# Kernel tuning notes

Hardware: AMD Instinct MI355X
Metric: run time of the kernel (lower is better)

The kernel has to match this reference:

```python
import jax, jax.numpy as jnp
import numpy as np

# Multi-scale feature pyramid (H, W) per level, standard Deformable-DETR for ~800x800 input
SHAPES = [(100, 100), (50, 50), (25, 25), (13, 13)]
D = 256      # d_model
NH = 8       # n_heads
NL = 4       # n_levels
NP = 4       # n_points
HD = D // NH # head_dim = 32
B = 2
S = sum(h * w for h, w in SHAPES)  # 13294
Lq = S  # encoder-style: one query per multi-scale token


def setup_inputs() -> dict:
    key = jax.random.key(0)
    ks = jax.random.split(key, 11)
    return {
        "query": jax.random.normal(ks[0], (B, Lq, D), jnp.float32),
        "reference_points": jax.random.uniform(ks[1], (B, Lq, NL, 2), jnp.float32),
        "value": jax.random.normal(ks[2], (B, S, D), jnp.float32),
        "W_val": jax.random.normal(ks[3], (D, D), jnp.float32) * 0.02,
        "b_val": jnp.zeros((D,), jnp.float32),
        "W_off": jax.random.normal(ks[4], (D, NH * NL * NP * 2), jnp.float32) * 0.01,
        "b_off": jax.random.normal(ks[5], (NH * NL * NP * 2,), jnp.float32) * 0.5,
        "W_attn": jax.random.normal(ks[6], (D, NH * NL * NP), jnp.float32) * 0.02,
        "b_attn": jnp.zeros((NH * NL * NP,), jnp.float32),
        "W_out": jax.random.normal(ks[7], (D, D), jnp.float32) * 0.02,
        "b_out": jnp.zeros((D,), jnp.float32),
    }


def _bilinear_sample(valf, x, y, H, W):
    """grid_sample(mode=bilinear, padding_mode=zeros, align_corners=False).
    valf: [N, H*W, C] flattened feature map; x, y: [N, P] pixel-space coords
    (already converted via x = loc_x*W - 0.5). Returns [N, P, C].
    """
    x0 = jnp.floor(x); y0 = jnp.floor(y)
    x1 = x0 + 1.0;     y1 = y0 + 1.0
    wx1 = x - x0; wx0 = 1.0 - wx1
    wy1 = y - y0; wy0 = 1.0 - wy1

    def corner(xi, yi, w):
        inb = (xi >= 0) & (xi <= W - 1) & (yi >= 0) & (yi <= H - 1)
        xi_c = jnp.clip(xi, 0, W - 1).astype(jnp.int32)
        yi_c = jnp.clip(yi, 0, H - 1).astype(jnp.int32)
        idx = yi_c * W + xi_c                                   # [N, P]
        v = jnp.take_along_axis(valf, idx[..., None], axis=1)   # [N, P, C]
        return v * (w * inb.astype(valf.dtype))[..., None]

    return (corner(x0, y0, wx0 * wy0) + corner(x1, y0, wx1 * wy0)
            + corner(x0, y1, wx0 * wy1) + corner(x1, y1, wx1 * wy1))


def reference(query, reference_points, value, W_val, b_val, W_off, b_off,
              W_attn, b_attn, W_out, b_out):
    Bq, L, _ = query.shape
    # value projection, split into heads: [B, S, NH, HD]
    val = (value @ W_val + b_val).reshape(Bq, S, NH, HD)
    # sampling offsets and attention weights from query
    offsets = (query @ W_off + b_off).reshape(Bq, L, NH, NL, NP, 2)
    w = (query @ W_attn + b_attn).reshape(Bq, L, NH, NL * NP)
    w = jax.nn.softmax(w, axis=-1).reshape(Bq, L, NH, NL, NP)
    # normalize offsets by (W, H) per level; 2D reference points path
    offset_norm = jnp.array([[wd, h] for h, wd in SHAPES], jnp.float32)  # [NL, 2]
    locs = (reference_points[:, :, None, :, None, :]
            + offsets / offset_norm[None, None, None, :, None, :])       # [B,L,NH,NL,NP,2]

    splits = [h * wd for h, wd in SHAPES]
    starts = np.concatenate([[0], np.cumsum(splits)])
    out_acc = jnp.zeros((Bq, L, NH, HD), query.dtype)
    for lvl, (H, W) in enumerate(SHAPES):
        vl = val[:, starts[lvl]:starts[lvl + 1]]                 # [B, HW, NH, HD]
        vl = vl.transpose(0, 2, 1, 3).reshape(Bq * NH, H * W, HD)
        loc = locs[:, :, :, lvl].transpose(0, 2, 1, 3, 4).reshape(Bq * NH, L * NP, 2)
        x = loc[..., 0] * W - 0.5   # align_corners=False pixel coords
        y = loc[..., 1] * H - 0.5
        s = _bilinear_sample(vl, x, y, H, W).reshape(Bq, NH, L, NP, HD)
        wl = w[:, :, :, lvl].transpose(0, 2, 1, 3)               # [B, NH, L, NP]
        out_acc = out_acc + jnp.einsum('bhqpd,bhqp->bqhd', s, wl)
    out = out_acc.reshape(Bq, L, NH * HD)
    return out @ W_out + b_out
```

## Files before the change

### kernel.cpp

```cpp
#include <hip/hip_runtime.h>
#include <hip/hip_bf16.h>
#include <math.h>

#define B_    2
#define D_    256
#define NH_   8
#define NL_   4
#define NP_   4
#define HD_   32
#define S_    13294
#define L_    13294
#define M_    (B_ * L_)

__device__ __constant__ int c_H[NL_]     = {100, 50, 25, 13};
__device__ __constant__ int c_W[NL_]     = {100, 50, 25, 13};
__device__ __constant__ int c_start[NL_] = {0, 10000, 12500, 13125};

typedef __attribute__((ext_vector_type(8))) short  short8;
typedef __attribute__((ext_vector_type(4))) float  float4v;

__device__ __forceinline__ unsigned short f2bf(float f) {
    unsigned u = __float_as_uint(f);
    unsigned r = 0x7fffu + ((u >> 16) & 1u);
    return (unsigned short)((u + r) >> 16);
}
__device__ __forceinline__ float bflo(int u) {
    return __uint_as_float((unsigned)u << 16);
}
__device__ __forceinline__ float bfhi(int u) {
    return __uint_as_float((unsigned)u & 0xffff0000u);
}

__global__ __launch_bounds__(256) void prep_weights(
    const float* __restrict__ W_val, const float* __restrict__ W_off,
    const float* __restrict__ W_attn, const float* __restrict__ b_off,
    const float* __restrict__ b_attn, const float* __restrict__ W_out,
    unsigned short* __restrict__ wt_val, unsigned short* __restrict__ wt_oa,
    unsigned short* __restrict__ wt_out, float* __restrict__ bias_oa)
{
    int i = blockIdx.x * 256 + threadIdx.x;
    if (i < 65536) {
        int n = i >> 8, k = i & 255;
        wt_val[i] = f2bf(W_val[k * 256 + n]);
    } else if (i < 65536 + 98304) {
        int j = i - 65536;
        int n = j >> 8, k = j & 255;
        float v = (n < 256) ? W_off[k * 256 + n] : W_attn[k * 128 + (n - 256)];
        wt_oa[j] = f2bf(v);
    } else if (i < 65536 + 98304 + 65536) {
        int j = i - 163840;
        int n = j >> 8, k = j & 255;
        wt_out[j] = f2bf(W_out[k * 256 + n]);
    } else if (i < 229376 + 384) {
        int j = i - 229376;
        bias_oa[j] = (j < 256) ? b_off[j] : b_attn[j - 256];
    }
}

template <bool A_F32, bool OUT_BF16>
__global__ __launch_bounds__(256) void gemm_mfma(
    const void* __restrict__ Av,
    const unsigned short* __restrict__ WT,
    const float* __restrict__ bias,
    void* __restrict__ Cv,
    int M, int N)
{
    __shared__ unsigned short As[128][40];
    __shared__ unsigned short Bs[128][40];

    const int tid  = threadIdx.x;
    const int lane = tid & 63;
    const int wave = tid >> 6;
    const int rowBase = blockIdx.x * 128;
    const int colBase = blockIdx.y * 128;
    const int wm = (wave >> 1) * 64;
    const int wn = (wave & 1) * 64;

    float4v acc[4][4] = {};

    const int fr = lane & 15;
    const int fk = (lane >> 4) * 8;

    for (int k0 = 0; k0 < 256; k0 += 32) {
        __syncthreads();
#pragma unroll
        for (int i = 0; i < 2; ++i) {
            const int c  = tid + i * 256;
            const int r  = c >> 2;
            const int ko = (c & 3) * 8;
            const int gr = rowBase + r;
            short8 va = {};
            if (gr < M) {
                if constexpr (A_F32) {
                    const float* Ap = (const float*)Av + (size_t)gr * 256 + k0 + ko;
                    float4 f0 = *reinterpret_cast<const float4*>(Ap);
                    float4 f1 = *reinterpret_cast<const float4*>(Ap + 4);
                    va[0] = (short)f2bf(f0.x); va[1] = (short)f2bf(f0.y);
                    va[2] = (short)f2bf(f0.z); va[3] = (short)f2bf(f0.w);
                    va[4] = (short)f2bf(f1.x); va[5] = (short)f2bf(f1.y);
                    va[6] = (short)f2bf(f1.z); va[7] = (short)f2bf(f1.w);
                } else {
                    va = *reinterpret_cast<const short8*>(
                        (const unsigned short*)Av + (size_t)gr * 256 + k0 + ko);
                }
            }
            *reinterpret_cast<short8*>(&As[r][ko]) = va;
            const int gc = colBase + r;
            short8 vb = *reinterpret_cast<const short8*>(WT + (size_t)gc * 256 + k0 + ko);
            *reinterpret_cast<short8*>(&Bs[r][ko]) = vb;
        }
        __syncthreads();

        short8 af[4], bf[4];
#pragma unroll
        for (int t = 0; t < 4; ++t) {
            af[t] = *reinterpret_cast<const short8*>(&As[wm + t * 16 + fr][fk]);
            bf[t] = *reinterpret_cast<const short8*>(&Bs[wn + t * 16 + fr][fk]);
        }
#pragma unroll
        for (int mt = 0; mt < 4; ++mt)
#pragma unroll
            for (int nt = 0; nt < 4; ++nt)
                acc[mt][nt] = __builtin_amdgcn_mfma_f32_16x16x32_bf16(
                    af[mt], bf[nt], acc[mt][nt], 0, 0, 0);
    }

    const int dn  = lane & 15;
    const int dm0 = (lane >> 4) * 4;
#pragma unroll
    for (int mt = 0; mt < 4; ++mt) {
#pragma unroll
        for (int nt = 0; nt < 4; ++nt) {
            const int col = colBase + wn + nt * 16 + dn;
            const float bv = bias[col];
#pragma unroll
            for (int r = 0; r < 4; ++r) {
                const int row = rowBase + wm + mt * 16 + dm0 + r;
                if (row < M) {
                    const float v = acc[mt][nt][r] + bv;
                    if constexpr (OUT_BF16)
                        ((unsigned short*)Cv)[(size_t)row * N + col] = f2bf(v);
                    else
                        ((float*)Cv)[(size_t)row * N + col] = v;
                }
            }
        }
    }
}

__global__ __launch_bounds__(256) void deform_sample_v2(
    const unsigned short* __restrict__ val,
    const float* __restrict__ refp,
    const float* __restrict__ oa,
    unsigned short* __restrict__ acc)
{
    const int tid = threadIdx.x;
    const int q0  = blockIdx.x * 8;

    __shared__ float sLog[8][128];
    __shared__ int2  sPack[8][4][16][9];

    {
        const int q  = tid >> 5;
        const int f  = tid & 31;
        const int bq = min(q0 + q, M_ - 1);
        float4 v = *reinterpret_cast<const float4*>(oa + (size_t)bq * 384 + 256 + f * 4);
        *reinterpret_cast<float4*>(&sLog[q][f * 4]) = v;
    }
    __syncthreads();

#pragma unroll
    for (int k = 0; k < 4; ++k) {
        const int e   = tid + k * 256;
        const int q   = e >> 7;
        const int t   = e & 127;
        const int h   = t >> 4;
        const int lp  = t & 15;
        const int lvl = lp >> 2;
        const int p   = lp & 3;
        const int bq  = min(q0 + q, M_ - 1);

        float m = -1e30f;
#pragma unroll
        for (int i = 0; i < 16; ++i) m = fmaxf(m, sLog[q][h * 16 + i]);
        float s = 0.f;
#pragma unroll
        for (int i = 0; i < 16; ++i) s += __expf(sLog[q][h * 16 + i] - m);
        const float wgt = __expf(sLog[q][t] - m) / s;

        const int Wi = c_W[lvl], Hi = c_H[lvl], st = c_start[lvl];
        const float rx = refp[((size_t)bq * NL_ + lvl) * 2 + 0];
        const float ry = refp[((size_t)bq * NL_ + lvl) * 2 + 1];
        const float ox = oa[(size_t)bq * 384 + h * 32 + lvl * 8 + p * 2 + 0];
        const float oy = oa[(size_t)bq * 384 + h * 32 + lvl * 8 + p * 2 + 1];
        const float x = rx * (float)Wi + ox - 0.5f;
        const float y = ry * (float)Hi + oy - 0.5f;

        const float x0f = floorf(x), y0f = floorf(y);
        const int   x0 = (int)x0f,   y0 = (int)y0f;
        const float wx1 = x - x0f, wx0 = 1.f - wx1;
        const float wy1 = y - y0f, wy0 = 1.f - wy1;

        const int   cx[4] = {x0, x0 + 1, x0,     x0 + 1};
        const int   cy[4] = {y0, y0,     y0 + 1, y0 + 1};
        const float cw[4] = {wx0 * wy0, wx1 * wy0, wx0 * wy1, wx1 * wy1};
#pragma unroll
        for (int c = 0; c < 4; ++c) {
            const bool inb = (cx[c] >= 0) & (cx[c] < Wi) & (cy[c] >= 0) & (cy[c] < Hi);
            const int xi = min(max(cx[c], 0), Wi - 1);
            const int yi = min(max(cy[c], 0), Hi - 1);
            int2 pk;
            pk.x = st + yi * Wi + xi;
            pk.y = __float_as_int(inb ? wgt * cw[c] : 0.f);
            sPack[q][c][lp][h] = pk;
        }
    }
    __syncthreads();

    const int q  = tid >> 5;
    const int h  = (tid >> 2) & 7;
    const int d4 = tid & 3;
    const int bq = q0 + q;
    const int b  = min(bq, M_ - 1) / L_;
    const unsigned short* vb = val + (size_t)b * S_ * 256 + h * 32 + d4 * 8;

    float a0 = 0, a1 = 0, a2 = 0, a3 = 0, a4 = 0, a5 = 0, a6 = 0, a7 = 0;
#pragma unroll 4
    for (int lp = 0; lp < 16; ++lp) {
#pragma unroll
        for (int c = 0; c < 4; ++c) {
            const int2 pk = sPack[q][c][lp][h];
            const float w = __int_as_float(pk.y);
            const int4 u = *reinterpret_cast<const int4*>(vb + (size_t)pk.x * 256);
            a0 += w * bflo(u.x); a1 += w * bfhi(u.x);
            a2 += w * bflo(u.y); a3 += w * bfhi(u.y);
            a4 += w * bflo(u.z); a5 += w * bfhi(u.z);
            a6 += w * bflo(u.w); a7 += w * bfhi(u.w);
        }
    }
    if (bq < M_) {
        int4 o;
        o.x = (int)f2bf(a0) | ((int)f2bf(a1) << 16);
        o.y = (int)f2bf(a2) | ((int)f2bf(a3) << 16);
        o.z = (int)f2bf(a4) | ((int)f2bf(a5) << 16);
        o.w = (int)f2bf(a6) | ((int)f2bf(a7) << 16);
        *reinterpret_cast<int4*>(acc + (size_t)bq * 256 + h * 32 + d4 * 8) = o;
    }
}

extern "C" void kernel_launch(void* const* d_in, const int* in_sizes, int n_in,
                              void* d_out, int out_size, void* d_ws, size_t ws_size,
                              hipStream_t stream) {
    const float* query  = (const float*)d_in[0];
    const float* refp   = (const float*)d_in[1];
    const float* value  = (const float*)d_in[2];
    const float* W_val  = (const float*)d_in[3];
    const float* b_val  = (const float*)d_in[4];
    const float* W_off  = (const float*)d_in[5];
    const float* b_off  = (const float*)d_in[6];
    const float* W_attn = (const float*)d_in[7];
    const float* b_attn = (const float*)d_in[8];
    const float* W_out  = (const float*)d_in[9];
    const float* b_out  = (const float*)d_in[10];
    float* out = (float*)d_out;

    char* ws = (char*)d_ws;
    const size_t mb = (size_t)M_ * 256;
    unsigned short* val_bf  = (unsigned short*)ws;  ws += mb * 2;
    unsigned short* acc_bf  = (unsigned short*)ws;  ws += mb * 2;
    float*          oa_f    = (float*)ws;           ws += (size_t)M_ * 384 * 4;
    unsigned short* wt_val  = (unsigned short*)ws;  ws += 65536 * 2;
    unsigned short* wt_oa   = (unsigned short*)ws;  ws += 98304 * 2;
    unsigned short* wt_out  = (unsigned short*)ws;  ws += 65536 * 2;
    float*          bias_oa = (float*)ws;           ws += 384 * 4;

    const int M = M_;
    dim3 blk(256);

    prep_weights<<<dim3(898), blk, 0, stream>>>(
        W_val, W_off, W_attn, b_off, b_attn, W_out, wt_val, wt_oa, wt_out, bias_oa);

    const dim3 gV((M + 127) / 128, 2);
    const dim3 gOA((M + 127) / 128, 3);

    gemm_mfma<true, true><<<gV, blk, 0, stream>>>(value, wt_val, b_val, val_bf, M, 256);
    gemm_mfma<true, false><<<gOA, blk, 0, stream>>>(query, wt_oa, bias_oa, oa_f, M, 384);
    deform_sample_v2<<<dim3((M + 7) / 8), blk, 0, stream>>>(val_bf, refp, oa_f, acc_bf);
    gemm_mfma<false, false><<<gV, blk, 0, stream>>>(acc_bf, wt_out, b_out, out, M, 256);
}
```

Measured before the change: 240.0 us.

## Merge value and offset GEMMs into one launch, shrink tiles, pack sample weights as fp16

The value-projection and offset/attention GEMMs now run as a single launch whose grid y-dimension selects the problem. Column tiles shrink from 128 to 64, which doubles the block count. In the sampling kernel the per-head softmax max and sum are computed once per (query, head) instead of once per sample point. Each sample index and its weight are packed into one 32-bit word with the weight stored as fp16, which halves shared-memory traffic but lowers weight precision. The smaller GEMM tiles re-read the A operand more often and give less reuse per block.

```diff
diff --git a/kernel.cpp b/kernel.cpp
--- a/kernel.cpp
+++ b/kernel.cpp
@@ -24,11 +24,15 @@
     unsigned r = 0x7fffu + ((u >> 16) & 1u);
     return (unsigned short)((u + r) >> 16);
 }
-__device__ __forceinline__ float bflo(int u) {
-    return __uint_as_float((unsigned)u << 16);
-}
-__device__ __forceinline__ float bfhi(int u) {
-    return __uint_as_float((unsigned)u & 0xffff0000u);
+__device__ __forceinline__ float bflo(int u) { return __uint_as_float((unsigned)u << 16); }
+__device__ __forceinline__ float bfhi(int u) { return __uint_as_float((unsigned)u & 0xffff0000u); }
+__device__ __forceinline__ unsigned short f2h(float f) {
+    _Float16 h = (_Float16)f;
+    return __builtin_bit_cast(unsigned short, h);
+}
+__device__ __forceinline__ float h2f(unsigned short u) {
+    _Float16 h = __builtin_bit_cast(_Float16, u);
+    return (float)h;
 }
 
 __global__ __launch_bounds__(256) void prep_weights(
@@ -57,27 +61,33 @@
     }
 }
 
-template <bool A_F32, bool OUT_BF16>
-__global__ __launch_bounds__(256) void gemm_mfma(
-    const void* __restrict__ Av,
-    const unsigned short* __restrict__ WT,
-    const float* __restrict__ bias,
-    void* __restrict__ Cv,
-    int M, int N)
+__global__ __launch_bounds__(256) void gemm_fused(
+    const float* __restrict__ value, const float* __restrict__ query,
+    const unsigned short* __restrict__ wt_val, const unsigned short* __restrict__ wt_oa,
+    const float* __restrict__ b_val, const float* __restrict__ bias_oa,
+    unsigned short* __restrict__ val_bf, float* __restrict__ oa_f)
 {
     __shared__ unsigned short As[128][40];
-    __shared__ unsigned short Bs[128][40];
+    __shared__ unsigned short Bs[64][40];
 
     const int tid  = threadIdx.x;
     const int lane = tid & 63;
     const int wave = tid >> 6;
     const int rowBase = blockIdx.x * 128;
-    const int colBase = blockIdx.y * 128;
+    const int y = blockIdx.y;
+
+    const float* A;
+    const unsigned short* WT;
+    const float* bias;
+    int N, colBase;
+    bool outBF16;
+    if (y < 4) { A = value; WT = wt_val; bias = b_val;   N = 256; colBase = y * 64;      outBF16 = true;  }
+    else       { A = query; WT = wt_oa;  bias = bias_oa; N = 384; colBase = (y - 4) * 64; outBF16 = false; }
+
     const int wm = (wave >> 1) * 64;
-    const int wn = (wave & 1) * 64;
-
-    float4v acc[4][4] = {};
-
+    const int wn = (wave & 1) * 32;
+
+    float4v acc[4][2] = {};
     const int fr = lane & 15;
     const int fk = (lane >> 4) * 8;
 
@@ -90,37 +100,119 @@
             const int ko = (c & 3) * 8;
             const int gr = rowBase + r;
             short8 va = {};
-            if (gr < M) {
-                if constexpr (A_F32) {
-                    const float* Ap = (const float*)Av + (size_t)gr * 256 + k0 + ko;
-                    float4 f0 = *reinterpret_cast<const float4*>(Ap);
-                    float4 f1 = *reinterpret_cast<const float4*>(Ap + 4);
-                    va[0] = (short)f2bf(f0.x); va[1] = (short)f2bf(f0.y);
-                    va[2] = (short)f2bf(f0.z); va[3] = (short)f2bf(f0.w);
-                    va[4] = (short)f2bf(f1.x); va[5] = (short)f2bf(f1.y);
-                    va[6] = (short)f2bf(f1.z); va[7] = (short)f2bf(f1.w);
-                } else {
-                    va = *reinterpret_cast<const short8*>(
-                        (const unsigned short*)Av + (size_t)gr * 256 + k0 + ko);
+            if (gr < M_) {
+                const float* Ap = A + (size_t)gr * 256 + k0 + ko;
+                float4 f0 = *reinterpret_cast<const float4*>(Ap);
+                float4 f1 = *reinterpret_cast<const float4*>(Ap + 4);
+                va[0] = (short)f2bf(f0.x); va[1] = (short)f2bf(f0.y);
+                va[2] = (short)f2bf(f0.z); va[3] = (short)f2bf(f0.w);
+                va[4] = (short)f2bf(f1.x); va[5] = (short)f2bf(f1.y);
+                va[6] = (short)f2bf(f1.z); va[7] = (short)f2bf(f1.w);
+            }
+            *reinterpret_cast<short8*>(&As[r][ko]) = va;
+        }
+        {
+            const int r  = tid >> 2;
+            const int ko = (tid & 3) * 8;
+            short8 vb = *reinterpret_cast<const short8*>(
+                WT + (size_t)(colBase + r) * 256 + k0 + ko);
+            *reinterpret_cast<short8*>(&Bs[r][ko]) = vb;
+        }
+        __syncthreads();
+
+        short8 af[4], bf[2];
+#pragma unroll
+        for (int t = 0; t < 4; ++t)
+            af[t] = *reinterpret_cast<const short8*>(&As[wm + t * 16 + fr][fk]);
+#pragma unroll
+        for (int t = 0; t < 2; ++t)
+            bf[t] = *reinterpret_cast<const short8*>(&Bs[wn + t * 16 + fr][fk]);
+#pragma unroll
+        for (int mt = 0; mt < 4; ++mt)
+#pragma unroll
+            for (int nt = 0; nt < 2; ++nt)
+                acc[mt][nt] = __builtin_amdgcn_mfma_f32_16x16x32_bf16(
+                    af[mt], bf[nt], acc[mt][nt], 0, 0, 0);
+    }
+
+    const int dn  = lane & 15;
+    const int dm0 = (lane >> 4) * 4;
+#pragma unroll
+    for (int mt = 0; mt < 4; ++mt) {
+#pragma unroll
+        for (int nt = 0; nt < 2; ++nt) {
+            const int col = colBase + wn + nt * 16 + dn;
+            const float bv = bias[col];
+#pragma unroll
+            for (int r = 0; r < 4; ++r) {
+                const int row = rowBase + wm + mt * 16 + dm0 + r;
+                if (row < M_) {
+                    const float v = acc[mt][nt][r] + bv;
+                    if (outBF16)
+                        val_bf[(size_t)row * 256 + col] = f2bf(v);
+                    else
+                        oa_f[(size_t)row * 384 + col] = v;
                 }
             }
+        }
+    }
+}
+
+__global__ __launch_bounds__(256) void gemm_out(
+    const unsigned short* __restrict__ Abf,
+    const unsigned short* __restrict__ WT,
+    const float* __restrict__ bias,
+    float* __restrict__ C)
+{
+    __shared__ unsigned short As[128][40];
+    __shared__ unsigned short Bs[64][40];
+
+    const int tid  = threadIdx.x;
+    const int lane = tid & 63;
+    const int wave = tid >> 6;
+    const int rowBase = blockIdx.x * 128;
+    const int colBase = blockIdx.y * 64;
+
+    const int wm = (wave >> 1) * 64;
+    const int wn = (wave & 1) * 32;
+
+    float4v acc[4][2] = {};
+    const int fr = lane & 15;
+    const int fk = (lane >> 4) * 8;
+
+    for (int k0 = 0; k0 < 256; k0 += 32) {
+        __syncthreads();
+#pragma unroll
+        for (int i = 0; i < 2; ++i) {
+            const int c  = tid + i * 256;
+            const int r  = c >> 2;
+            const int ko = (c & 3) * 8;
+            const int gr = rowBase + r;
+            short8 va = {};
+            if (gr < M_)
+                va = *reinterpret_cast<const short8*>(Abf + (size_t)gr * 256 + k0 + ko);
             *reinterpret_cast<short8*>(&As[r][ko]) = va;
-            const int gc = colBase + r;
-            short8 vb = *reinterpret_cast<const short8*>(WT + (size_t)gc * 256 + k0 + ko);
+        }
+        {
+            const int r  = tid >> 2;
+            const int ko = (tid & 3) * 8;
+            short8 vb = *reinterpret_cast<const short8*>(
+                WT + (size_t)(colBase + r) * 256 + k0 + ko);
             *reinterpret_cast<short8*>(&Bs[r][ko]) = vb;
         }
         __syncthreads();
 
-        short8 af[4], bf[4];
-#pragma unroll
-        for (int t = 0; t < 4; ++t) {
+        short8 af[4], bf[2];
+#pragma unroll
+        for (int t = 0; t < 4; ++t)
             af[t] = *reinterpret_cast<const short8*>(&As[wm + t * 16 + fr][fk]);
+#pragma unroll
+        for (int t = 0; t < 2; ++t)
             bf[t] = *reinterpret_cast<const short8*>(&Bs[wn + t * 16 + fr][fk]);
-        }
 #pragma unroll
         for (int mt = 0; mt < 4; ++mt)
 #pragma unroll
-            for (int nt = 0; nt < 4; ++nt)
+            for (int nt = 0; nt < 2; ++nt)
                 acc[mt][nt] = __builtin_amdgcn_mfma_f32_16x16x32_bf16(
                     af[mt], bf[nt], acc[mt][nt], 0, 0, 0);
     }
@@ -130,25 +222,20 @@
 #pragma unroll
     for (int mt = 0; mt < 4; ++mt) {
 #pragma unroll
-        for (int nt = 0; nt < 4; ++nt) {
+        for (int nt = 0; nt < 2; ++nt) {
             const int col = colBase + wn + nt * 16 + dn;
             const float bv = bias[col];
 #pragma unroll
             for (int r = 0; r < 4; ++r) {
                 const int row = rowBase + wm + mt * 16 + dm0 + r;
-                if (row < M) {
-                    const float v = acc[mt][nt][r] + bv;
-                    if constexpr (OUT_BF16)
-                        ((unsigned short*)Cv)[(size_t)row * N + col] = f2bf(v);
-                    else
-                        ((float*)Cv)[(size_t)row * N + col] = v;
-                }
+                if (row < M_)
+                    C[(size_t)row * 256 + col] = acc[mt][nt][r] + bv;
             }
         }
     }
 }
 
-__global__ __launch_bounds__(256) void deform_sample_v2(
+__global__ __launch_bounds__(256) void deform_sample_v3(
     const unsigned short* __restrict__ val,
     const float* __restrict__ refp,
     const float* __restrict__ oa,
@@ -158,7 +245,8 @@
     const int q0  = blockIdx.x * 8;
 
     __shared__ float sLog[8][128];
-    __shared__ int2  sPack[8][4][16][9];
+    __shared__ float sMS[8][8][2];
+    __shared__ int   sPack[8][4][16][8];
 
     {
         const int q  = tid >> 5;
@@ -166,6 +254,19 @@
         const int bq = min(q0 + q, M_ - 1);
         float4 v = *reinterpret_cast<const float4*>(oa + (size_t)bq * 384 + 256 + f * 4);
         *reinterpret_cast<float4*>(&sLog[q][f * 4]) = v;
+    }
+    __syncthreads();
+
+    if (tid < 64) {
+        const int q = tid >> 3, h = tid & 7;
+        float m = -1e30f;
+#pragma unroll
+        for (int i = 0; i < 16; ++i) m = fmaxf(m, sLog[q][h * 16 + i]);
+        float s = 0.f;
+#pragma unroll
+        for (int i = 0; i < 16; ++i) s += __expf(sLog[q][h * 16 + i] - m);
+        sMS[q][h][0] = m;
+        sMS[q][h][1] = 1.f / s;
     }
     __syncthreads();
 
@@ -180,13 +281,7 @@
         const int p   = lp & 3;
         const int bq  = min(q0 + q, M_ - 1);
 
-        float m = -1e30f;
-#pragma unroll
-        for (int i = 0; i < 16; ++i) m = fmaxf(m, sLog[q][h * 16 + i]);
-        float s = 0.f;
-#pragma unroll
-        for (int i = 0; i < 16; ++i) s += __expf(sLog[q][h * 16 + i] - m);
-        const float wgt = __expf(sLog[q][t] - m) / s;
+        const float wgt = __expf(sLog[q][t] - sMS[q][h][0]) * sMS[q][h][1];
 
         const int Wi = c_W[lvl], Hi = c_H[lvl], st = c_start[lvl];
         const float rx = refp[((size_t)bq * NL_ + lvl) * 2 + 0];
@@ -209,10 +304,9 @@
             const bool inb = (cx[c] >= 0) & (cx[c] < Wi) & (cy[c] >= 0) & (cy[c] < Hi);
             const int xi = min(max(cx[c], 0), Wi - 1);
             const int yi = min(max(cy[c], 0), Hi - 1);
-            int2 pk;
-            pk.x = st + yi * Wi + xi;
-            pk.y = __float_as_int(inb ? wgt * cw[c] : 0.f);
-            sPack[q][c][lp][h] = pk;
+            const int idx = st + yi * Wi + xi;
+            const unsigned short wh = f2h(inb ? wgt * cw[c] : 0.f);
+            sPack[q][c][lp][h] = idx | ((int)wh << 16);
         }
     }
     __syncthreads();
@@ -225,18 +319,18 @@
     const unsigned short* vb = val + (size_t)b * S_ * 256 + h * 32 + d4 * 8;
 
     float a0 = 0, a1 = 0, a2 = 0, a3 = 0, a4 = 0, a5 = 0, a6 = 0, a7 = 0;
-#pragma unroll 4
-    for (int lp = 0; lp < 16; ++lp) {
-#pragma unroll
-        for (int c = 0; c < 4; ++c) {
-            const int2 pk = sPack[q][c][lp][h];
-            const float w = __int_as_float(pk.y);
-            const int4 u = *reinterpret_cast<const int4*>(vb + (size_t)pk.x * 256);
-            a0 += w * bflo(u.x); a1 += w * bfhi(u.x);
-            a2 += w * bflo(u.y); a3 += w * bfhi(u.y);
-            a4 += w * bflo(u.z); a5 += w * bfhi(u.z);
-            a6 += w * bflo(u.w); a7 += w * bfhi(u.w);
-        }
+#pragma unroll 8
+    for (int i = 0; i < 64; ++i) {
+        const int lp = i >> 2;
+        const int c  = i & 3;
+        const int pk = sPack[q][c][lp][h];
+        const float w = h2f((unsigned short)((unsigned)pk >> 16));
+        const unsigned idx = (unsigned)pk & 0xffffu;
+        const int4 u = *reinterpret_cast<const int4*>(vb + (size_t)idx * 256);
+        a0 += w * bflo(u.x); a1 += w * bfhi(u.x);
+        a2 += w * bflo(u.y); a3 += w * bfhi(u.y);
+        a4 += w * bflo(u.z); a5 += w * bfhi(u.z);
+        a6 += w * bflo(u.w); a7 += w * bfhi(u.w);
     }
     if (bq < M_) {
         int4 o;
@@ -274,17 +368,15 @@
     unsigned short* wt_out  = (unsigned short*)ws;  ws += 65536 * 2;
     float*          bias_oa = (float*)ws;           ws += 384 * 4;
 
-    const int M = M_;
     dim3 blk(256);
 
     prep_weights<<<dim3(898), blk, 0, stream>>>(
         W_val, W_off, W_attn, b_off, b_attn, W_out, wt_val, wt_oa, wt_out, bias_oa);
 
-    const dim3 gV((M + 127) / 128, 2);
-    const dim3 gOA((M + 127) / 128, 3);
-
-    gemm_mfma<true, true><<<gV, blk, 0, stream>>>(value, wt_val, b_val, val_bf, M, 256);
-    gemm_mfma<true, false><<<gOA, blk, 0, stream>>>(query, wt_oa, bias_oa, oa_f, M, 384);
-    deform_sample_v2<<<dim3((M + 7) / 8), blk, 0, stream>>>(val_bf, refp, oa_f, acc_bf);
-    gemm_mfma<false, false><<<gV, blk, 0, stream>>>(acc_bf, wt_out, b_out, out, M, 256);
-}
+    gemm_fused<<<dim3((M_ + 127) / 128, 10), blk, 0, stream>>>(
+        value, query, wt_val, wt_oa, b_val, bias_oa, val_bf, oa_f);
+
+    deform_sample_v3<<<dim3((M_ + 7) / 8), blk, 0, stream>>>(val_bf, refp, oa_f, acc_bf);
+
+    gemm_out<<<dim3((M_ + 127) / 128, 4), blk, 0, stream>>>(acc_bf, wt_out, b_out, out);
+}
```

Measured after the change: 212.2 us. 11.6% less time.

## Merge value/query GEMMs, register-prefetch tiles, fp16 value and packed sample indices

Applied to the files above, without the earlier changes.

The value and offset/attention projections now run in one launch, with a 64-row tile that covers the full output width. A register-prefetched loop loads the next K-slice while the MFMAs run on the current one. The value projection is stored as fp16 instead of bf16. The sampling kernel computes the softmax max and sum once per head rather than once per thread, and packs the 16-bit index with an fp16 weight into one int so the LDS table is smaller. fp16 value storage can overflow or lose range compared with bf16, and the 16-bit index only holds because S is below 65536.

```diff
diff --git a/kernel.cpp b/kernel.cpp
--- a/kernel.cpp
+++ b/kernel.cpp
@@ -3,14 +3,13 @@
 #include <math.h>
 
 #define B_    2
-#define D_    256
 #define NH_   8
 #define NL_   4
 #define NP_   4
 #define HD_   32
 #define S_    13294
 #define L_    13294
-#define M_    (B_ * L_)
+#define M_    26588
 
 __device__ __constant__ int c_H[NL_]     = {100, 50, 25, 13};
 __device__ __constant__ int c_W[NL_]     = {100, 50, 25, 13};
@@ -24,11 +23,13 @@
     unsigned r = 0x7fffu + ((u >> 16) & 1u);
     return (unsigned short)((u + r) >> 16);
 }
-__device__ __forceinline__ float bflo(int u) {
-    return __uint_as_float((unsigned)u << 16);
-}
-__device__ __forceinline__ float bfhi(int u) {
-    return __uint_as_float((unsigned)u & 0xffff0000u);
+__device__ __forceinline__ unsigned short f2h(float f) {
+    _Float16 h = (_Float16)f;
+    return __builtin_bit_cast(unsigned short, h);
+}
+__device__ __forceinline__ float h2f(unsigned short u) {
+    _Float16 h = __builtin_bit_cast(_Float16, u);
+    return (float)h;
 }
 
 __global__ __launch_bounds__(256) void prep_weights(
@@ -57,98 +58,151 @@
     }
 }
 
-template <bool A_F32, bool OUT_BF16>
-__global__ __launch_bounds__(256) void gemm_mfma(
+template<int N, int OUT, bool AF32>
+__device__ __forceinline__ void gemm_body(
     const void* __restrict__ Av,
     const unsigned short* __restrict__ WT,
     const float* __restrict__ bias,
     void* __restrict__ Cv,
-    int M, int N)
-{
-    __shared__ unsigned short As[128][40];
-    __shared__ unsigned short Bs[128][40];
+    unsigned short (* __restrict__ As)[40],
+    unsigned short (* __restrict__ Bs)[40])
+{
+    constexpr int NT  = N / 64;
+    constexpr int NCH = N / 64;
 
     const int tid  = threadIdx.x;
     const int lane = tid & 63;
     const int wave = tid >> 6;
-    const int rowBase = blockIdx.x * 128;
-    const int colBase = blockIdx.y * 128;
-    const int wm = (wave >> 1) * 64;
-    const int wn = (wave & 1) * 64;
-
-    float4v acc[4][4] = {};
+    const int rowBase = blockIdx.x * 64;
+    const int wcol = wave * (N / 4);
+
+    const int ar   = tid >> 2;
+    const int ako  = (tid & 3) * 8;
+    const int grow = rowBase + ar;
+
+    float4v acc[4][NT] = {};
+    float4 pa0, pa1;
+    short8 pah;
+    short8 pb[NCH];
+
+    auto loadAB = [&](int k0) {
+        if constexpr (AF32) {
+            const float* A = (const float*)Av;
+            if (grow < M_) {
+                pa0 = *reinterpret_cast<const float4*>(A + (size_t)grow * 256 + k0 + ako);
+                pa1 = *reinterpret_cast<const float4*>(A + (size_t)grow * 256 + k0 + ako + 4);
+            } else {
+                pa0 = make_float4(0.f, 0.f, 0.f, 0.f); pa1 = pa0;
+            }
+        } else {
+            const unsigned short* A = (const unsigned short*)Av;
+            if (grow < M_)
+                pah = *reinterpret_cast<const short8*>(A + (size_t)grow * 256 + k0 + ako);
+            else
+                pah = short8{};
+        }
+#pragma unroll
+        for (int i = 0; i < NCH; ++i) {
+            const int c = tid + i * 256;
+            pb[i] = *reinterpret_cast<const short8*>(
+                WT + (size_t)(c >> 2) * 256 + k0 + (c & 3) * 8);
+        }
+    };
+
+    auto storeLDS = [&]() {
+        short8 s;
+        if constexpr (AF32) {
+            s[0] = (short)f2bf(pa0.x); s[1] = (short)f2bf(pa0.y);
+            s[2] = (short)f2bf(pa0.z); s[3] = (short)f2bf(pa0.w);
+            s[4] = (short)f2bf(pa1.x); s[5] = (short)f2bf(pa1.y);
+            s[6] = (short)f2bf(pa1.z); s[7] = (short)f2bf(pa1.w);
+        } else {
+            s = pah;
+        }
+        *reinterpret_cast<short8*>(&As[ar][ako]) = s;
+#pragma unroll
+        for (int i = 0; i < NCH; ++i) {
+            const int c = tid + i * 256;
+            *reinterpret_cast<short8*>(&Bs[c >> 2][(c & 3) * 8]) = pb[i];
+        }
+    };
 
     const int fr = lane & 15;
     const int fk = (lane >> 4) * 8;
 
-    for (int k0 = 0; k0 < 256; k0 += 32) {
+    loadAB(0);
+#pragma unroll
+    for (int it = 0; it < 8; ++it) {
         __syncthreads();
-#pragma unroll
-        for (int i = 0; i < 2; ++i) {
-            const int c  = tid + i * 256;
-            const int r  = c >> 2;
-            const int ko = (c & 3) * 8;
-            const int gr = rowBase + r;
-            short8 va = {};
-            if (gr < M) {
-                if constexpr (A_F32) {
-                    const float* Ap = (const float*)Av + (size_t)gr * 256 + k0 + ko;
-                    float4 f0 = *reinterpret_cast<const float4*>(Ap);
-                    float4 f1 = *reinterpret_cast<const float4*>(Ap + 4);
-                    va[0] = (short)f2bf(f0.x); va[1] = (short)f2bf(f0.y);
-                    va[2] = (short)f2bf(f0.z); va[3] = (short)f2bf(f0.w);
-                    va[4] = (short)f2bf(f1.x); va[5] = (short)f2bf(f1.y);
-                    va[6] = (short)f2bf(f1.z); va[7] = (short)f2bf(f1.w);
-                } else {
-                    va = *reinterpret_cast<const short8*>(
-                        (const unsigned short*)Av + (size_t)gr * 256 + k0 + ko);
+        storeLDS();
+        __syncthreads();
+        if (it < 7) loadAB((it + 1) * 32);
+
+        short8 af[4], bf[NT];
+#pragma unroll
+        for (int t = 0; t < 4; ++t)
+            af[t] = *reinterpret_cast<const short8*>(&As[t * 16 + fr][fk]);
+#pragma unroll
+        for (int t = 0; t < NT; ++t)
+            bf[t] = *reinterpret_cast<const short8*>(&Bs[wcol + t * 16 + fr][fk]);
+#pragma unroll
+        for (int mt = 0; mt < 4; ++mt)
+#pragma unroll
+            for (int nt = 0; nt < NT; ++nt)
+                acc[mt][nt] = __builtin_amdgcn_mfma_f32_16x16x32_bf16(
+                    af[mt], bf[nt], acc[mt][nt], 0, 0, 0);
+    }
+
+    const int dn  = lane & 15;
+    const int dm0 = (lane >> 4) * 4;
+#pragma unroll
+    for (int mt = 0; mt < 4; ++mt) {
+#pragma unroll
+        for (int nt = 0; nt < NT; ++nt) {
+            const int col = wcol + nt * 16 + dn;
+            const float bv = bias[col];
+#pragma unroll
+            for (int r = 0; r < 4; ++r) {
+                const int row = rowBase + mt * 16 + dm0 + r;
+                if (row < M_) {
+                    const float v = acc[mt][nt][r] + bv;
+                    if constexpr (OUT == 0)
+                        ((unsigned short*)Cv)[(size_t)row * 256 + col] = f2h(v);
+                    else if constexpr (OUT == 1)
+                        ((float*)Cv)[(size_t)row * 384 + col] = v;
+                    else
+                        ((float*)Cv)[(size_t)row * 256 + col] = v;
                 }
             }
-            *reinterpret_cast<short8*>(&As[r][ko]) = va;
-            const int gc = colBase + r;
-            short8 vb = *reinterpret_cast<const short8*>(WT + (size_t)gc * 256 + k0 + ko);
-            *reinterpret_cast<short8*>(&Bs[r][ko]) = vb;
-        }
-        __syncthreads();
-
-        short8 af[4], bf[4];
-#pragma unroll
-        for (int t = 0; t < 4; ++t) {
-            af[t] = *reinterpret_cast<const short8*>(&As[wm + t * 16 + fr][fk]);
-            bf[t] = *reinterpret_cast<const short8*>(&Bs[wn + t * 16 + fr][fk]);
-        }
-#pragma unroll
-        for (int mt = 0; mt < 4; ++mt)
-#pragma unroll
-            for (int nt = 0; nt < 4; ++nt)
-                acc[mt][nt] = __builtin_amdgcn_mfma_f32_16x16x32_bf16(
-                    af[mt], bf[nt], acc[mt][nt], 0, 0, 0);
-    }
-
-    const int dn  = lane & 15;
-    const int dm0 = (lane >> 4) * 4;
-#pragma unroll
-    for (int mt = 0; mt < 4; ++mt) {
-#pragma unroll
-        for (int nt = 0; nt < 4; ++nt) {
-            const int col = colBase + wn + nt * 16 + dn;
-            const float bv = bias[col];
-#pragma unroll
-            for (int r = 0; r < 4; ++r) {
-                const int row = rowBase + wm + mt * 16 + dm0 + r;
-                if (row < M) {
-                    const float v = acc[mt][nt][r] + bv;
-                    if constexpr (OUT_BF16)
-                        ((unsigned short*)Cv)[(size_t)row * N + col] = f2bf(v);
-                    else
-                        ((float*)Cv)[(size_t)row * N + col] = v;
-                }
-            }
-        }
-    }
-}
-
-__global__ __launch_bounds__(256) void deform_sample_v2(
+        }
+    }
+}
+
+__global__ __launch_bounds__(256) void gemm_vq(
+    const float* __restrict__ value, const float* __restrict__ query,
+    const unsigned short* __restrict__ wt_val, const unsigned short* __restrict__ wt_oa,
+    const float* __restrict__ b_val, const float* __restrict__ bias_oa,
+    unsigned short* __restrict__ val_f16, float* __restrict__ oa_f)
+{
+    __shared__ unsigned short As[64][40];
+    __shared__ unsigned short Bs[384][40];
+    if (blockIdx.y == 0)
+        gemm_body<256, 0, true>(value, wt_val, b_val, val_f16, As, Bs);
+    else
+        gemm_body<384, 1, true>(query, wt_oa, bias_oa, oa_f, As, Bs);
+}
+
+__global__ __launch_bounds__(256) void gemm_out2(
+    const unsigned short* __restrict__ Abf,
+    const unsigned short* __restrict__ WT,
+    const float* __restrict__ bias, float* __restrict__ C)
+{
+    __shared__ unsigned short As[64][40];
+    __shared__ unsigned short Bs[256][40];
+    gemm_body<256, 2, false>(Abf, WT, bias, C, As, Bs);
+}
+
+__global__ __launch_bounds__(256) void deform_sample_v4(
     const unsigned short* __restrict__ val,
     const float* __restrict__ refp,
     const float* __restrict__ oa,
@@ -158,7 +212,8 @@
     const int q0  = blockIdx.x * 8;
 
     __shared__ float sLog[8][128];
-    __shared__ int2  sPack[8][4][16][9];
+    __shared__ float sMS[8][8][2];
+    __shared__ int   sPack[8][4][16][8];
 
     {
         const int q  = tid >> 5;
@@ -166,6 +221,19 @@
         const int bq = min(q0 + q, M_ - 1);
         float4 v = *reinterpret_cast<const float4*>(oa + (size_t)bq * 384 + 256 + f * 4);
         *reinterpret_cast<float4*>(&sLog[q][f * 4]) = v;
+    }
+    __syncthreads();
+
+    if (tid < 64) {
+        const int q = tid >> 3, h = tid & 7;
+        float m = -1e30f;
+#pragma unroll
+        for (int i = 0; i < 16; ++i) m = fmaxf(m, sLog[q][h * 16 + i]);
+        float s = 0.f;
+#pragma unroll
+        for (int i = 0; i < 16; ++i) s += __expf(sLog[q][h * 16 + i] - m);
+        sMS[q][h][0] = m;
+        sMS[q][h][1] = 1.f / s;
     }
     __syncthreads();
 
@@ -180,13 +248,7 @@
         const int p   = lp & 3;
         const int bq  = min(q0 + q, M_ - 1);
 
-        float m = -1e30f;
-#pragma unroll
-        for (int i = 0; i < 16; ++i) m = fmaxf(m, sLog[q][h * 16 + i]);
-        float s = 0.f;
-#pragma unroll
-        for (int i = 0; i < 16; ++i) s += __expf(sLog[q][h * 16 + i] - m);
-        const float wgt = __expf(sLog[q][t] - m) / s;
+        const float wgt = __expf(sLog[q][t] - sMS[q][h][0]) * sMS[q][h][1];
 
         const int Wi = c_W[lvl], Hi = c_H[lvl], st = c_start[lvl];
         const float rx = refp[((size_t)bq * NL_ + lvl) * 2 + 0];
@@ -209,10 +271,9 @@
             const bool inb = (cx[c] >= 0) & (cx[c] < Wi) & (cy[c] >= 0) & (cy[c] < Hi);
             const int xi = min(max(cx[c], 0), Wi - 1);
             const int yi = min(max(cy[c], 0), Hi - 1);
-            int2 pk;
-            pk.x = st + yi * Wi + xi;
-            pk.y = __float_as_int(inb ? wgt * cw[c] : 0.f);
-            sPack[q][c][lp][h] = pk;
+            const int idx = st + yi * Wi + xi;
+            const unsigned short wh = f2h(inb ? wgt * cw[c] : 0.f);
+            sPack[q][c][lp][h] = idx | ((int)wh << 16);
         }
     }
     __syncthreads();
@@ -225,18 +286,22 @@
     const unsigned short* vb = val + (size_t)b * S_ * 256 + h * 32 + d4 * 8;
 
     float a0 = 0, a1 = 0, a2 = 0, a3 = 0, a4 = 0, a5 = 0, a6 = 0, a7 = 0;
-#pragma unroll 4
-    for (int lp = 0; lp < 16; ++lp) {
-#pragma unroll
-        for (int c = 0; c < 4; ++c) {
-            const int2 pk = sPack[q][c][lp][h];
-            const float w = __int_as_float(pk.y);
-            const int4 u = *reinterpret_cast<const int4*>(vb + (size_t)pk.x * 256);
-            a0 += w * bflo(u.x); a1 += w * bfhi(u.x);
-            a2 += w * bflo(u.y); a3 += w * bfhi(u.y);
-            a4 += w * bflo(u.z); a5 += w * bfhi(u.z);
-            a6 += w * bflo(u.w); a7 += w * bfhi(u.w);
-        }
+#pragma unroll 8
+    for (int i = 0; i < 64; ++i) {
+        const int lp = i >> 2;
+        const int c  = i & 3;
+        const int pk = sPack[q][c][lp][h];
+        const float w = h2f((unsigned short)((unsigned)pk >> 16));
+        const unsigned idx = (unsigned)pk & 0xffffu;
+        const int4 u = *reinterpret_cast<const int4*>(vb + (size_t)idx * 256);
+        a0 += w * h2f((unsigned short)(u.x & 0xffff));
+        a1 += w * h2f((unsigned short)((unsigned)u.x >> 16));
+        a2 += w * h2f((unsigned short)(u.y & 0xffff));
+        a3 += w * h2f((unsigned short)((unsigned)u.y >> 16));
+        a4 += w * h2f((unsigned short)(u.z & 0xffff));
+        a5 += w * h2f((unsigned short)((unsigned)u.z >> 16));
+        a6 += w * h2f((unsigned short)(u.w & 0xffff));
+        a7 += w * h2f((unsigned short)((unsigned)u.w >> 16));
     }
     if (bq < M_) {
         int4 o;
@@ -266,7 +331,7 @@
 
     char* ws = (char*)d_ws;
     const size_t mb = (size_t)M_ * 256;
-    unsigned short* val_bf  = (unsigned short*)ws;  ws += mb * 2;
+    unsigned short* val_f16 = (unsigned short*)ws;  ws += mb * 2;
     unsigned short* acc_bf  = (unsigned short*)ws;  ws += mb * 2;
     float*          oa_f    = (float*)ws;           ws += (size_t)M_ * 384 * 4;
     unsigned short* wt_val  = (unsigned short*)ws;  ws += 65536 * 2;
@@ -274,17 +339,15 @@
     unsigned short* wt_out  = (unsigned short*)ws;  ws += 65536 * 2;
     float*          bias_oa = (float*)ws;           ws += 384 * 4;
 
-    const int M = M_;
     dim3 blk(256);
 
     prep_weights<<<dim3(898), blk, 0, stream>>>(
         W_val, W_off, W_attn, b_off, b_attn, W_out, wt_val, wt_oa, wt_out, bias_oa);
 
-    const dim3 gV((M + 127) / 128, 2);
-    const dim3 gOA((M + 127) / 128, 3);
-
-    gemm_mfma<true, true><<<gV, blk, 0, stream>>>(value, wt_val, b_val, val_bf, M, 256);
-    gemm_mfma<true, false><<<gOA, blk, 0, stream>>>(query, wt_oa, bias_oa, oa_f, M, 384);
-    deform_sample_v2<<<dim3((M + 7) / 8), blk, 0, stream>>>(val_bf, refp, oa_f, acc_bf);
-    gemm_mfma<false, false><<<gV, blk, 0, stream>>>(acc_bf, wt_out, b_out, out, M, 256);
-}
+    gemm_vq<<<dim3((M_ + 63) / 64, 2), blk, 0, stream>>>(
+        value, query, wt_val, wt_oa, b_val, bias_oa, val_f16, oa_f);
+
+    deform_sample_v4<<<dim3((M_ + 7) / 8), blk, 0, stream>>>(val_f16, refp, oa_f, acc_bf);
+
+    gemm_out2<<<dim3((M_ + 63) / 64), blk, 0, stream>>>(acc_bf, wt_out, b_out, out);
+}
```

Result: faster. 207.6 us (-13.5%).
